# Kernel tuning notes

Hardware: AMD Instinct MI355X
Metric: run time of the kernel (lower is better)

## Reference

```python
import jax, jax.numpy as jnp
import numpy as np

B, S, D = 2048, 200, 192  # batch, seq_len, total_dim
H1, H2 = 64, 32
IN = 4 * D


def prelu(x, a):
    return jnp.where(x >= 0, x, a * x)


def setup_inputs() -> dict:
    key = jax.random.key(0)
    ks = jax.random.split(key, 10)
    scale = lambda fan_in: 1.0 / np.sqrt(fan_in)
    return {
        "query": jax.random.normal(ks[0], (B, D), jnp.float32),
        "keys": jax.random.normal(ks[1], (B, S, D), jnp.float32),
        "keys_mask": jax.random.randint(ks[2], (B, S), 0, 2, jnp.int32),
        "W1": jax.random.uniform(ks[3], (IN, H1), jnp.float32, -scale(IN), scale(IN)),
        "b1": jnp.zeros((H1,), jnp.float32),
        "a1": jnp.asarray(0.25, jnp.float32),  # PReLU default slope
        "W2": jax.random.uniform(ks[4], (H1, H2), jnp.float32, -scale(H1), scale(H1)),
        "b2": jnp.zeros((H2,), jnp.float32),
        "a2": jnp.asarray(0.25, jnp.float32),
        "W3": jax.random.uniform(ks[5], (H2, 1), jnp.float32, -scale(H2), scale(H2)),
        "b3": jnp.zeros((1,), jnp.float32),
    }


def reference(query, keys, keys_mask, W1, b1, a1, W2, b2, a2, W3, b3):
    q = query[:, None, :]  # [B,1,D] broadcasts against keys [B,S,D]
    qe = jnp.broadcast_to(q, keys.shape)
    x = jnp.concatenate([keys, qe, keys * qe, keys - qe], axis=-1)  # [B,S,4D]
    h = prelu(jnp.einsum("bsi,ih->bsh", x, W1) + b1, a1)
    h = prelu(jnp.einsum("bsh,hk->bsk", h, W2) + b2, a2)
    scores = (jnp.einsum("bsk,ko->bso", h, W3) + b3)[..., 0]  # [B,S]
    scores = jnp.where(keys_mask.astype(bool), scores, -jnp.inf)
    w = jax.nn.softmax(scores, axis=-1)
    w = jnp.where(jnp.isnan(w), jnp.zeros_like(w), w)
    weighted_sum = jnp.einsum("bs,bsd->bd", w, keys)
    return weighted_sum, w
```

## Files before the change

kernel.cpp:

```cpp
#include <hip/hip_runtime.h>


#define B_N 2048
#define S_N 200
#define D_N 192

typedef __bf16 bf16x8 __attribute__((ext_vector_type(8)));
typedef __bf16 bf16x4 __attribute__((ext_vector_type(4)));
typedef float  f32x4  __attribute__((ext_vector_type(4)));

__device__ __forceinline__ float rfl(float x) {
  return __uint_as_float(__builtin_amdgcn_readfirstlane(__float_as_uint(x)));
}

struct __align__(16) Smem {
  unsigned char kbuf[64*400];
  union {
    unsigned char h1buf[64*144];
    unsigned char w2t[32*144];
  };
  union {
    float qbuf[192];
    float scores[256];
  };
  float cbuf[64];
  union {
    float cpart[4][64];
    float opart[4][192];
  };
  unsigned char maskbuf[256];
  float wm[4], wl[4];
  float w3buf[32];
  float b2buf[32];
  float consts[4];
};

__global__ __launch_bounds__(256, 4) void rich_attn_kernel(
    const float* __restrict__ query, const float* __restrict__ keys,
    const int*   __restrict__ keys_mask, const float* __restrict__ W1,
    const float* __restrict__ b1, const float* __restrict__ a1,
    const float* __restrict__ W2, const float* __restrict__ b2,
    const float* __restrict__ a2, const float* __restrict__ W3,
    const float* __restrict__ b3, float* __restrict__ out)
{
  __shared__ Smem sm;
  const int tid  = threadIdx.x;
  const int b    = blockIdx.x;
  const int wave = tid >> 6;
  const int lane = tid & 63;
  const int quad = (tid >> 4) & 3;
  const int n16  = tid & 15;

  if (tid < 192) sm.qbuf[tid] = query[b*D_N + tid];
  sm.maskbuf[tid] = (tid < 200) ? (unsigned char)(keys_mask[b*S_N + tid] != 0) : 0;
  if (tid < 32)  sm.w3buf[tid] = W3[tid];
  else if (tid < 64) sm.b2buf[tid-32] = b2[tid-32];
  if (tid == 64) { sm.consts[0] = a1[0]; sm.consts[1] = a2[0]; sm.consts[2] = b3[0]; }
  for (int i = tid; i < 64*32; i += 256) {
    int hh = i >> 5, kk = i & 31;
    *((__bf16*)&sm.w2t[kk*144 + hh*2]) = (__bf16)W2[i];
  }
  __syncthreads();

  {
    int hh = tid & 63, pp = tid >> 6;
    float acc = 0.f;
    int d0 = pp*48;
    #pragma unroll 4
    for (int d = d0; d < d0+48; ++d)
      acc += sm.qbuf[d] * (W1[(192+d)*64 + hh] - W1[(576+d)*64 + hh]);
    sm.cpart[pp][hh] = acc;
  }
  bf16x8 fb1[6];
  {
    int h = (wave << 4) | n16;
    #pragma unroll
    for (int t = 0; t < 6; ++t) {
      #pragma unroll
      for (int jh = 0; jh < 2; ++jh) {
        #pragma unroll
        for (int j2 = 0; j2 < 4; ++j2) {
          int j = jh*4 + j2;
          int d = t*32 + quad*8 + j;
          float v = W1[d*64 + h] + W1[(576+d)*64 + h] + sm.qbuf[d]*W1[(384+d)*64 + h];
          fb1[t][j] = (__bf16)v;
        }
        __builtin_amdgcn_sched_barrier(0);
      }
    }
  }
  bf16x8 fw2[2][2];
  #pragma unroll
  for (int nt2 = 0; nt2 < 2; ++nt2)
    #pragma unroll
    for (int t = 0; t < 2; ++t)
      fw2[nt2][t] = *(const bf16x8*)&sm.w2t[(nt2*16 + n16)*144 + (t*32 + quad*8)*2];
  const float w3v0 = sm.w3buf[n16],      w3v1 = sm.w3buf[16 + n16];
  const float bbv0 = sm.b2buf[n16],      bbv1 = sm.b2buf[16 + n16];
  const float a1v = rfl(sm.consts[0]), a2v = rfl(sm.consts[1]), b3v = rfl(sm.consts[2]);
  __syncthreads();
  if (tid < 64)
    sm.cbuf[tid] = b1[tid] + sm.cpart[0][tid] + sm.cpart[1][tid]
                 + sm.cpart[2][tid] + sm.cpart[3][tid];

  const float* kb = keys + (size_t)b * (S_N * D_N);
  float m_run = -1e30f, l_run = 0.f;
  f32x4 o = {0.f, 0.f, 0.f, 0.f};

  for (int tile = 0; tile < 4; ++tile) {
    const int s0 = tile * 64;
    #pragma unroll
    for (int ch = 0; ch < 3; ++ch) {
      float4 v[4];
      #pragma unroll
      for (int u = 0; u < 4; ++u) {
        int f = tid + (ch*4 + u)*256;
        int sg = s0 + f/48;
        v[u] = make_float4(0.f, 0.f, 0.f, 0.f);
        if (sg < 200) v[u] = ((const float4*)kb)[sg*48 + (f%48)];
      }
      #pragma unroll
      for (int u = 0; u < 4; ++u) {
        int f = tid + (ch*4 + u)*256;
        int row = f/48, c4 = f%48;
        bf16x4 bv;
        bv[0]=(__bf16)v[u].x; bv[1]=(__bf16)v[u].y;
        bv[2]=(__bf16)v[u].z; bv[3]=(__bf16)v[u].w;
        *(bf16x4*)&sm.kbuf[row*400 + c4*8] = bv;
      }
      __builtin_amdgcn_sched_barrier(0);
    }
    __syncthreads();

    {
      int h = (wave << 4) | n16;
      float cb = sm.cbuf[h];
      #pragma unroll
      for (int mt = 0; mt < 4; ++mt) {
        f32x4 acc1 = (f32x4){0.f,0.f,0.f,0.f};
        #pragma unroll
        for (int t = 0; t < 6; ++t) {
          bf16x8 fa = *(const bf16x8*)&sm.kbuf[(mt*16 + n16)*400 + (t*32 + quad*8)*2];
          acc1 = __builtin_amdgcn_mfma_f32_16x16x32_bf16(fa, fb1[t], acc1, 0, 0, 0);
        }
        #pragma unroll
        for (int r = 0; r < 4; ++r) {
          int m = mt*16 + quad*4 + r;
          float v = acc1[r] + cb;
          v = (v >= 0.f) ? v : a1v * v;
          *((__bf16*)&sm.h1buf[m*144 + h*2]) = (__bf16)v;
        }
        __builtin_amdgcn_sched_barrier(0);
      }
    }
    __syncthreads();

    bf16x8 fa2[2];
    #pragma unroll
    for (int t = 0; t < 2; ++t)
      fa2[t] = *(const bf16x8*)&sm.h1buf[(wave*16 + n16)*144 + (t*32 + quad*8)*2];
    f32x4 acc2[2];
    acc2[0] = (f32x4){0.f,0.f,0.f,0.f};
    acc2[1] = (f32x4){0.f,0.f,0.f,0.f};
    #pragma unroll
    for (int nt2 = 0; nt2 < 2; ++nt2)
      #pragma unroll
      for (int t = 0; t < 2; ++t)
        acc2[nt2] = __builtin_amdgcn_mfma_f32_16x16x32_bf16(fa2[t], fw2[nt2][t], acc2[nt2], 0, 0, 0);

    float sc[4];
    #pragma unroll
    for (int r = 0; r < 4; ++r) {
      float v0 = acc2[0][r] + bbv0; v0 = (v0 >= 0.f) ? v0 : a2v * v0;
      float v1 = acc2[1][r] + bbv1; v1 = (v1 >= 0.f) ? v1 : a2v * v1;
      sc[r] = v0 * w3v0 + v1 * w3v1;
    }
    #pragma unroll
    for (int off = 1; off < 16; off <<= 1)
      #pragma unroll
      for (int r = 0; r < 4; ++r) sc[r] += __shfl_xor(sc[r], off);

    float p[4];
    float mloc = -1e30f;
    #pragma unroll
    for (int r = 0; r < 4; ++r) {
      int sg = s0 + wave*16 + quad*4 + r;
      sc[r] += b3v;
      bool valid = (sg < 200) && (sm.maskbuf[sg] != 0);
      sc[r] = valid ? sc[r] : -1e30f;
      mloc = fmaxf(mloc, sc[r]);
    }
    if (n16 == 0) {
      #pragma unroll
      for (int r = 0; r < 4; ++r) sm.scores[s0 + wave*16 + quad*4 + r] = sc[r];
    }
    mloc = fmaxf(mloc, __shfl_xor(mloc, 16));
    mloc = fmaxf(mloc, __shfl_xor(mloc, 32));
    float m_new = fmaxf(m_run, mloc);
    float fac = __expf(m_run - m_new);
    float psum = 0.f;
    #pragma unroll
    for (int r = 0; r < 4; ++r) {
      p[r] = (sc[r] > -1e29f) ? __expf(sc[r] - m_new) : 0.f;
      psum += p[r];
    }
    psum += __shfl_xor(psum, 16);
    psum += __shfl_xor(psum, 32);
    l_run = l_run * fac + psum;
    m_run = m_new;

    o[0] *= fac; o[1] *= fac; o[2] *= fac; o[3] *= fac;
    #pragma unroll
    for (int s2 = 0; s2 < 16; ++s2) {
      float pvs = __shfl(p[s2 & 3], (s2 >> 2) * 16);
      if (lane < 48) {
        bf16x4 kv = *(const bf16x4*)&sm.kbuf[(wave*16 + s2)*400 + lane*8];
        o[0] += pvs * (float)kv[0];
        o[1] += pvs * (float)kv[1];
        o[2] += pvs * (float)kv[2];
        o[3] += pvs * (float)kv[3];
      }
    }
    __syncthreads();
  }

  if (lane == 0) { sm.wm[wave] = m_run; sm.wl[wave] = l_run; }
  if (lane < 48) *(f32x4*)&sm.opart[wave][lane*4] = o;
  __syncthreads();
  float mg = fmaxf(fmaxf(sm.wm[0], sm.wm[1]), fmaxf(sm.wm[2], sm.wm[3]));
  float e0 = __expf(sm.wm[0] - mg), e1 = __expf(sm.wm[1] - mg);
  float e2 = __expf(sm.wm[2] - mg), e3 = __expf(sm.wm[3] - mg);
  float lg = sm.wl[0]*e0 + sm.wl[1]*e1 + sm.wl[2]*e2 + sm.wl[3]*e3;
  float invl = (lg > 0.f) ? 1.f / lg : 0.f;
  if (tid < 192) {
    float os = sm.opart[0][tid]*e0 + sm.opart[1][tid]*e1
             + sm.opart[2][tid]*e2 + sm.opart[3][tid]*e3;
    out[(size_t)b * D_N + tid] = os * invl;
  }
  if (tid < 200) {
    float wv = (lg > 0.f) ? __expf(sm.scores[tid] - mg) * invl : 0.f;
    out[(size_t)B_N * D_N + (size_t)b * S_N + tid] = wv;
  }
}

extern "C" void kernel_launch(void* const* d_in, const int* in_sizes, int n_in,
                              void* d_out, int out_size, void* d_ws, size_t ws_size,
                              hipStream_t stream) {
  const float* query     = (const float*)d_in[0];
  const float* keys      = (const float*)d_in[1];
  const int*   keys_mask = (const int*)  d_in[2];
  const float* W1        = (const float*)d_in[3];
  const float* b1        = (const float*)d_in[4];
  const float* a1        = (const float*)d_in[5];
  const float* W2        = (const float*)d_in[6];
  const float* b2        = (const float*)d_in[7];
  const float* a2        = (const float*)d_in[8];
  const float* W3        = (const float*)d_in[9];
  const float* b3        = (const float*)d_in[10];
  float* out = (float*)d_out;
  rich_attn_kernel<<<dim3(B_N), dim3(256), 0, stream>>>(
      query, keys, keys_mask, W1, b1, a1, W2, b2, a2, W3, b3, out);
}
```

Before: 522.0 us.

## Prefetch next key tile into registers while computing current tile

Key loads move into a 12-float4 register buffer. The next tile's global loads are issued right after the barrier, so they overlap with the MLP and softmax compute on the current tile, and the first tile is issued before the weight setup. This adds 48 live VGPRs, so launch bounds drop from 4 to 3 blocks per CU to leave room, which trades occupancy for latency hiding. Some sched_barriers in the W1 fragment build and the h1 store loop are relaxed or removed.

```diff
diff --git a/kernel.cpp b/kernel.cpp
--- a/kernel.cpp
+++ b/kernel.cpp
@@ -35,7 +35,7 @@
   float consts[4];
 };
 
-__global__ __launch_bounds__(256, 4) void rich_attn_kernel(
+__global__ __launch_bounds__(256, 3) void rich_attn_kernel(
     const float* __restrict__ query, const float* __restrict__ keys,
     const int*   __restrict__ keys_mask, const float* __restrict__ W1,
     const float* __restrict__ b1, const float* __restrict__ a1,
@@ -51,6 +51,32 @@
   const int quad = (tid >> 4) & 3;
   const int n16  = tid & 15;
 
+  const float* kb = keys + (size_t)b * (S_N * D_N);
+
+  float4 v[12];
+  auto issue_tile = [&](int s0_) {
+    #pragma unroll
+    for (int u = 0; u < 12; ++u) {
+      int f = tid + u*256;
+      int sg = s0_ + f/48;
+      v[u] = make_float4(0.f, 0.f, 0.f, 0.f);
+      if (sg < 200) v[u] = ((const float4*)kb)[sg*48 + (f%48)];
+    }
+  };
+  auto write_tile = [&]() {
+    #pragma unroll
+    for (int u = 0; u < 12; ++u) {
+      int f = tid + u*256;
+      int row = f/48, c4 = f%48;
+      bf16x4 bv;
+      bv[0]=(__bf16)v[u].x; bv[1]=(__bf16)v[u].y;
+      bv[2]=(__bf16)v[u].z; bv[3]=(__bf16)v[u].w;
+      *(bf16x4*)&sm.kbuf[row*400 + c4*8] = bv;
+    }
+  };
+
+  issue_tile(0);
+
   if (tid < 192) sm.qbuf[tid] = query[b*D_N + tid];
   sm.maskbuf[tid] = (tid < 200) ? (unsigned char)(keys_mask[b*S_N + tid] != 0) : 0;
   if (tid < 32)  sm.w3buf[tid] = W3[tid];
@@ -77,16 +103,12 @@
     #pragma unroll
     for (int t = 0; t < 6; ++t) {
       #pragma unroll
-      for (int jh = 0; jh < 2; ++jh) {
-        #pragma unroll
-        for (int j2 = 0; j2 < 4; ++j2) {
-          int j = jh*4 + j2;
-          int d = t*32 + quad*8 + j;
-          float v = W1[d*64 + h] + W1[(576+d)*64 + h] + sm.qbuf[d]*W1[(384+d)*64 + h];
-          fb1[t][j] = (__bf16)v;
-        }
-        __builtin_amdgcn_sched_barrier(0);
+      for (int j = 0; j < 8; ++j) {
+        int d = t*32 + quad*8 + j;
+        float v1 = W1[d*64 + h] + W1[(576+d)*64 + h] + sm.qbuf[d]*W1[(384+d)*64 + h];
+        fb1[t][j] = (__bf16)v1;
       }
+      __builtin_amdgcn_sched_barrier(0);
     }
   }
   bf16x8 fw2[2][2];
@@ -103,34 +125,14 @@
     sm.cbuf[tid] = b1[tid] + sm.cpart[0][tid] + sm.cpart[1][tid]
                  + sm.cpart[2][tid] + sm.cpart[3][tid];
 
-  const float* kb = keys + (size_t)b * (S_N * D_N);
   float m_run = -1e30f, l_run = 0.f;
   f32x4 o = {0.f, 0.f, 0.f, 0.f};
 
   for (int tile = 0; tile < 4; ++tile) {
     const int s0 = tile * 64;
-    #pragma unroll
-    for (int ch = 0; ch < 3; ++ch) {
-      float4 v[4];
-      #pragma unroll
-      for (int u = 0; u < 4; ++u) {
-        int f = tid + (ch*4 + u)*256;
-        int sg = s0 + f/48;
-        v[u] = make_float4(0.f, 0.f, 0.f, 0.f);
-        if (sg < 200) v[u] = ((const float4*)kb)[sg*48 + (f%48)];
-      }
-      #pragma unroll
-      for (int u = 0; u < 4; ++u) {
-        int f = tid + (ch*4 + u)*256;
-        int row = f/48, c4 = f%48;
-        bf16x4 bv;
-        bv[0]=(__bf16)v[u].x; bv[1]=(__bf16)v[u].y;
-        bv[2]=(__bf16)v[u].z; bv[3]=(__bf16)v[u].w;
-        *(bf16x4*)&sm.kbuf[row*400 + c4*8] = bv;
-      }
-      __builtin_amdgcn_sched_barrier(0);
-    }
+    write_tile();
     __syncthreads();
+    if (tile < 3) issue_tile(s0 + 64);
 
     {
       int h = (wave << 4) | n16;
@@ -146,11 +148,10 @@
         #pragma unroll
         for (int r = 0; r < 4; ++r) {
           int m = mt*16 + quad*4 + r;
-          float v = acc1[r] + cb;
-          v = (v >= 0.f) ? v : a1v * v;
-          *((__bf16*)&sm.h1buf[m*144 + h*2]) = (__bf16)v;
+          float v1 = acc1[r] + cb;
+          v1 = (v1 >= 0.f) ? v1 : a1v * v1;
+          *((__bf16*)&sm.h1buf[m*144 + h*2]) = (__bf16)v1;
         }
-        __builtin_amdgcn_sched_barrier(0);
       }
     }
     __syncthreads();
```

Result: slower. 592.5 us (+13.5%).
